# Optimization experiments

Hardware: AMD Instinct MI355X
Metric: run time of the kernel (lower is better)

Reference implementation:

```python
import jax, jax.numpy as jnp
import numpy as np

VOXEL_LENGTH = 1.2


def grid_sample_3d_border(vol, grid):
    """torch.nn.functional.grid_sample (5D, bilinear, align_corners=False,
    padding_mode='border') with grid flattened to (B, N, 3) in (x, y, z) order.
    vol: (B, C, D, H, W). Returns (B, C, N)."""

    def sample_one(v, g):
        C, D, H, W = v.shape
        x, y, z = g[:, 0], g[:, 1], g[:, 2]
        # align_corners=False unnormalization
        ix = ((x + 1.0) * W - 1.0) * 0.5
        iy = ((y + 1.0) * H - 1.0) * 0.5
        iz = ((z + 1.0) * D - 1.0) * 0.5
        ix0f, iy0f, iz0f = jnp.floor(ix), jnp.floor(iy), jnp.floor(iz)
        wx, wy, wz = ix - ix0f, iy - iy0f, iz - iz0f
        # border padding: clamp indices, keep unclamped weights
        x0 = jnp.clip(ix0f, 0, W - 1).astype(jnp.int32)
        x1 = jnp.clip(ix0f + 1, 0, W - 1).astype(jnp.int32)
        y0 = jnp.clip(iy0f, 0, H - 1).astype(jnp.int32)
        y1 = jnp.clip(iy0f + 1, 0, H - 1).astype(jnp.int32)
        z0 = jnp.clip(iz0f, 0, D - 1).astype(jnp.int32)
        z1 = jnp.clip(iz0f + 1, 0, D - 1).astype(jnp.int32)
        vflat = v.reshape(C, D * H * W)

        def gather(zi, yi, xi):  # -> (C, N)
            return vflat[:, (zi * H + yi) * W + xi]

        out = (
            gather(z0, y0, x0) * ((1 - wz) * (1 - wy) * (1 - wx))
            + gather(z0, y0, x1) * ((1 - wz) * (1 - wy) * wx)
            + gather(z0, y1, x0) * ((1 - wz) * wy * (1 - wx))
            + gather(z0, y1, x1) * ((1 - wz) * wy * wx)
            + gather(z1, y0, x0) * (wz * (1 - wy) * (1 - wx))
            + gather(z1, y0, x1) * (wz * (1 - wy) * wx)
            + gather(z1, y1, x0) * (wz * wy * (1 - wx))
            + gather(z1, y1, x1) * (wz * wy * wx)
        )
        return out

    return jax.vmap(sample_one)(vol, grid)


def setup_inputs() -> dict:
    key = jax.random.key(0)
    ks = jax.random.split(key, 16)
    B, IMG, STEPS = 2, 64, 24
    N = IMG * IMG * STEPS
    C_IN, HID, RES = 32, 256, 32
    # points in world space, inside the voxel cube [-0.6, 0.6]
    points = jax.random.uniform(ks[0], (B, N, 3), jnp.float32) * 1.2 - 0.6
    feature_volume = jax.random.normal(ks[1], (B, C_IN, RES, RES, RES), jnp.float32)

    def lin(k, fan_in, fan_out, scale):
        kw, kb = jax.random.split(k)
        W = jax.random.uniform(kw, (fan_out, fan_in), jnp.float32, -scale, scale)
        b = jax.random.uniform(kb, (fan_out,), jnp.float32, -scale, scale)
        return W, b

    freq = 12.0
    W0, b0 = lin(ks[2], C_IN, HID, 1.0 / C_IN)  # first_layer_film_sine_init
    W1, b1 = lin(ks[3], HID, HID, float(np.sqrt(6.0 / HID) / freq))
    W2, b2 = lin(ks[4], HID, HID, float(np.sqrt(6.0 / HID) / freq))
    W3, b3 = lin(ks[5], HID, HID, float(np.sqrt(6.0 / HID) / freq))
    Wf, bf = lin(ks[6], HID, 4, float(np.sqrt(6.0 / HID) / freq))
    return {
        "points": points, "feature_volume": feature_volume,
        "W0": W0, "b0": b0, "W1": W1, "b1": b1, "W2": W2, "b2": b2,
        "W3": W3, "b3": b3, "Wf": Wf, "bf": bf,
        "img_size": 64, "num_steps": 24,
    }


def reference(points, feature_volume, W0, b0, W1, b1, W2, b2, W3, b3, Wf, bf,
              img_size, num_steps):
    grid = points / (VOXEL_LENGTH / 2.0)  # (B, N, 3) in [-1, 1]
    feats = grid_sample_3d_border(feature_volume, grid)  # (B, C, N)
    x = feats.transpose(0, 2, 1)  # (B, N, C)
    for W, b in ((W0, b0), (W1, b1), (W2, b2), (W3, b3)):
        x = jnp.sin(jnp.einsum('bnc,hc->bnh', x, W) + b)
    rgb_sigma = jnp.einsum('bnh,oh->bno', x, Wf) + bf  # (B, N, 4)
    rgb = jax.nn.sigmoid(rgb_sigma[..., :3])
    sigma = rgb_sigma[..., 3:4]
    return jnp.concatenate([rgb, sigma], axis=-1)
```

## Files before the change

kernel.cpp:

```cpp
#include <hip/hip_runtime.h>
#include <math.h>

#define THREADS 256

typedef __attribute__((ext_vector_type(8))) short bf16x8;
typedef __attribute__((ext_vector_type(4))) float f32x4;

#define STREAM_BYTES  458752

__device__ __host__ __forceinline__ int sigma_k(int k) {
    return (k & 0xE1) | ((k & 0x04) << 2) | ((k & 0x18) >> 1) | (k & 0x02);
}

__device__ __forceinline__ ushort f2bf(float f) {
    union { float f; unsigned u; } v; v.f = f;
    unsigned r = v.u + 0x7FFFu + ((v.u >> 16) & 1u);
    return (ushort)(r >> 16);
}

__device__ __forceinline__ float fast_sigmoid(float x) {
    return 1.0f / (1.0f + __expf(-x));
}

__device__ __forceinline__ unsigned cvt_pk_bf16(float lo, float hi) {
    unsigned d;
    asm("v_cvt_pk_bf16_f32 %0, %1, %2" : "=v"(d) : "v"(lo), "v"(hi));
    return d;
}

__global__ void build_frags(const float* __restrict__ W0,
                            const float* __restrict__ W1,
                            const float* __restrict__ W2,
                            const float* __restrict__ W3,
                            const float* __restrict__ Wf,
                            ushort* __restrict__ stream) {
    const int gid = blockIdx.x * 256 + threadIdx.x;
    const int f = gid >> 6;
    const int lane = gid & 63;
    const int p16 = lane & 15, g = lane >> 4;
    ushort* dst = stream + (size_t)f * 512 + lane * 8;

    if (f < 16) {
        const float* row = W0 + (size_t)(f * 16 + p16) * 32;
#pragma unroll
        for (int i = 0; i < 8; ++i) dst[i] = f2bf(row[8 * g + i]);
    } else if (f < 32) {
#pragma unroll
        for (int i = 0; i < 8; ++i) dst[i] = 0;
    } else if (f < 416) {
        const int t = f - 32;
        const int h = t >> 7;
        const int q = (t >> 5) & 3;
        const int ksl = (t >> 3) & 3;
        const int ntl = t & 7;
        const int nt = (q & 1) * 8 + ntl;
        const int ks = (q >> 1) * 4 + ksl;
        const float* W = (h == 0) ? W1 : (h == 1) ? W2 : W3;
        const float* row = W + (size_t)(nt * 16 + p16) * 256;
#pragma unroll
        for (int i = 0; i < 8; ++i) dst[i] = f2bf(row[sigma_k(32 * ks + 8 * g + i)]);
    } else if (f < 424) {
        const int ks = f - 416;
        if (p16 < 4) {
            const float* row = Wf + (size_t)p16 * 256;
#pragma unroll
            for (int i = 0; i < 8; ++i) dst[i] = f2bf(row[sigma_k(32 * ks + 8 * g + i)]);
        } else {
#pragma unroll
            for (int i = 0; i < 8; ++i) dst[i] = 0;
        }
    } else {
#pragma unroll
        for (int i = 0; i < 8; ++i) dst[i] = 0;
    }
}

__global__ void vol_chlast(const float* __restrict__ vol, float* __restrict__ dst, int nvox) {
    int v = blockIdx.x * 256 + threadIdx.x;
    if (v >= nvox) return;
    const int b = v >> 15, idx = v & 32767;
    const float* s = vol + (size_t)b * 32 * 32768 + idx;
    float* d = dst + (size_t)v * 32;
#pragma unroll
    for (int c = 0; c < 32; ++c) d[c] = s[(size_t)c * 32768];
}

#define MF(a, b, c) __builtin_amdgcn_mfma_f32_16x16x32_bf16((a), (b), (c), 0, 0, 0)

__global__ __launch_bounds__(THREADS, 2)
void siren_pl(const float* __restrict__ points,
              const float* __restrict__ vol,
              const float* __restrict__ b0, const float* __restrict__ b1,
              const float* __restrict__ b2, const float* __restrict__ b3,
              const float* __restrict__ bfin,
              const ushort* __restrict__ Wstream,
              const float* __restrict__ volcl, int use_cl,
              float* __restrict__ out, long long total, int N) {
    __shared__ ushort ring[2][16384];

    const int tid = (int)threadIdx.x;
    const int w = tid >> 6;
    const int lane = tid & 63;
    const int p16 = lane & 15;
    const int g = lane >> 4;

    const long long base = (long long)blockIdx.x * 128;

    auto stage = [&](int c) {
        if (c >= 14) return;
        const ushort* src = Wstream + (size_t)c * 16384;
        ushort* dstbase = &ring[c & 1][0];
#pragma unroll
        for (int q = 0; q < 8; ++q) {
            const int off = (q * 4 + w) * 512;
            __builtin_amdgcn_global_load_lds(
                (const __attribute__((address_space(1))) unsigned int*)(src + off + lane * 8),
                (__attribute__((address_space(3))) unsigned int*)(dstbase + off),
                16, 0, 0);
        }
    };
    stage(0);
    stage(1);

    bf16x8 af0[2];
    {
#pragma unroll
        for (int ptt = 0; ptt < 2; ++ptt) {
            const long long gidx = base + w * 32 + ptt * 16 + p16;
            const long long gp = gidx < total ? gidx : total - 1;
            const int bi = (int)(gp / N);
            const float* pp = points + gp * 3;
            const float sc = 1.0f / 0.6f;
            const float ix = (pp[0] * sc + 1.0f) * 16.0f - 0.5f;
            const float iy = (pp[1] * sc + 1.0f) * 16.0f - 0.5f;
            const float iz = (pp[2] * sc + 1.0f) * 16.0f - 0.5f;
            const float fx = floorf(ix), fy = floorf(iy), fz = floorf(iz);
            const float wx = ix - fx, wy = iy - fy, wz = iz - fz;
            const int x0 = (int)fminf(fmaxf(fx, 0.0f), 31.0f);
            const int x1 = (int)fminf(fmaxf(fx + 1.0f, 0.0f), 31.0f);
            const int y0 = (int)fminf(fmaxf(fy, 0.0f), 31.0f);
            const int y1 = (int)fminf(fmaxf(fy + 1.0f, 0.0f), 31.0f);
            const int z0 = (int)fminf(fmaxf(fz, 0.0f), 31.0f);
            const int z1 = (int)fminf(fmaxf(fz + 1.0f, 0.0f), 31.0f);
            const int i000 = (z0 * 32 + y0) * 32 + x0, i001 = (z0 * 32 + y0) * 32 + x1;
            const int i010 = (z0 * 32 + y1) * 32 + x0, i011 = (z0 * 32 + y1) * 32 + x1;
            const int i100 = (z1 * 32 + y0) * 32 + x0, i101 = (z1 * 32 + y0) * 32 + x1;
            const int i110 = (z1 * 32 + y1) * 32 + x0, i111 = (z1 * 32 + y1) * 32 + x1;
            const float omx = 1.0f - wx, omy = 1.0f - wy, omz = 1.0f - wz;
            const float w000 = omz * omy * omx, w001 = omz * omy * wx;
            const float w010 = omz * wy * omx,  w011 = omz * wy * wx;
            const float w100 = wz * omy * omx,  w101 = wz * omy * wx;
            const float w110 = wz * wy * omx,   w111 = wz * wy * wx;

            f32x4 a[2];
            if (use_cl) {
                const float* vb = volcl + (size_t)bi * 32768 * 32 + g * 8;
#pragma unroll
                for (int h = 0; h < 2; ++h) {
                    const float* vh = vb + h * 4;
                    a[h]  = w000 * *(const f32x4*)(vh + (size_t)i000 * 32);
                    a[h] += w001 * *(const f32x4*)(vh + (size_t)i001 * 32);
                    a[h] += w010 * *(const f32x4*)(vh + (size_t)i010 * 32);
                    a[h] += w011 * *(const f32x4*)(vh + (size_t)i011 * 32);
                    a[h] += w100 * *(const f32x4*)(vh + (size_t)i100 * 32);
                    a[h] += w101 * *(const f32x4*)(vh + (size_t)i101 * 32);
                    a[h] += w110 * *(const f32x4*)(vh + (size_t)i110 * 32);
                    a[h] += w111 * *(const f32x4*)(vh + (size_t)i111 * 32);
                }
            } else {
                const float* vb = vol + ((size_t)bi * 32 + (size_t)g * 8) * 32768;
#pragma unroll
                for (int c = 0; c < 8; ++c) {
                    const float* vc = vb + (size_t)c * 32768;
                    a[c >> 2][c & 3] =
                        vc[i000] * w000 + vc[i001] * w001 + vc[i010] * w010 + vc[i011] * w011 +
                        vc[i100] * w100 + vc[i101] * w101 + vc[i110] * w110 + vc[i111] * w111;
                }
            }
            union { bf16x8 v; unsigned u[4]; } pk;
            pk.u[0] = cvt_pk_bf16(a[0][0], a[0][1]);
            pk.u[1] = cvt_pk_bf16(a[0][2], a[0][3]);
            pk.u[2] = cvt_pk_bf16(a[1][0], a[1][1]);
            pk.u[3] = cvt_pk_bf16(a[1][2], a[1][3]);
            af0[ptt] = pk.v;
        }
    }

    f32x4 accA[2][8];
    f32x4 accB[2][8];
    bf16x8 bfr[2][8];

    auto frag_at = [&](int slot, int idx) -> bf16x8 {
        return *(const bf16x8*)&ring[slot][idx * 512 + lane * 8];
    };
    auto init_half = [&](f32x4 (&A)[2][8], const float* __restrict__ b, int ntbase) {
#pragma unroll
        for (int m = 0; m < 8; ++m) {
            const f32x4 bv = *(const f32x4*)&b[(ntbase + m) * 16 + 4 * g];
            A[0][m] = bv; A[1][m] = bv;
        }
    };
    auto pack_half = [&](f32x4 (&A)[2][8], int ksbase) {
#pragma unroll
        for (int ptt = 0; ptt < 2; ++ptt)
#pragma unroll
            for (int ks2 = 0; ks2 < 4; ++ks2) {
                union { bf16x8 v; unsigned u[4]; } pk;
#pragma unroll
                for (int j = 0; j < 4; ++j) {
                    const int m = 2 * ks2 + (j >> 1);
                    const int r = 2 * (j & 1);
                    pk.u[j] = cvt_pk_bf16(__sinf(A[ptt][m][r]), __sinf(A[ptt][m][r + 1]));
                }
                bfr[ptt][ksbase + ks2] = pk.v;
            }
    };
    auto chunk_mfma = [&](int slot, int kh, f32x4 (&A)[2][8]) {
        __builtin_amdgcn_s_setprio(1);
#pragma unroll
        for (int ksl = 0; ksl < 4; ++ksl) {
            const bf16x8 bA = bfr[0][kh * 4 + ksl];
            const bf16x8 bB = bfr[1][kh * 4 + ksl];
#pragma unroll
            for (int ntl = 0; ntl < 8; ++ntl) {
                const bf16x8 wfr = frag_at(slot, ksl * 8 + ntl);
                A[0][ntl] = MF(wfr, bA, A[0][ntl]);
                A[1][ntl] = MF(wfr, bB, A[1][ntl]);
            }
        }
        __builtin_amdgcn_s_setprio(0);
    };

    init_half(accA, b0, 0);
    init_half(accB, b0, 8);
    __syncthreads();

    __builtin_amdgcn_s_setprio(1);
#pragma unroll
    for (int ntl = 0; ntl < 8; ++ntl) {
        const bf16x8 wl = frag_at(0, ntl);
        const bf16x8 wh = frag_at(0, 8 + ntl);
        accA[0][ntl] = MF(wl, af0[0], accA[0][ntl]);
        accA[1][ntl] = MF(wl, af0[1], accA[1][ntl]);
        accB[0][ntl] = MF(wh, af0[0], accB[0][ntl]);
        accB[1][ntl] = MF(wh, af0[1], accB[1][ntl]);
    }
    __builtin_amdgcn_s_setprio(0);
    __syncthreads(); stage(2);

    pack_half(accA, 0); init_half(accA, b1, 0);
    chunk_mfma(1, 0, accA);
    __syncthreads(); stage(3);
    pack_half(accB, 4); init_half(accB, b1, 8);
    chunk_mfma(0, 0, accB);
    __syncthreads(); stage(4);
    chunk_mfma(1, 1, accA);
    __syncthreads(); stage(5);
    pack_half(accA, 0); init_half(accA, b2, 0);
    chunk_mfma(0, 1, accB);
    __syncthreads(); stage(6);
    pack_half(accB, 4); init_half(accB, b2, 8);
    chunk_mfma(1, 0, accA);
    __syncthreads(); stage(7);
    chunk_mfma(0, 0, accB);
    __syncthreads(); stage(8);
    chunk_mfma(1, 1, accA);
    __syncthreads(); stage(9);
    pack_half(accA, 0); init_half(accA, b3, 0);
    chunk_mfma(0, 1, accB);
    __syncthreads(); stage(10);
    pack_half(accB, 4); init_half(accB, b3, 8);
    chunk_mfma(1, 0, accA);
    __syncthreads(); stage(11);
    chunk_mfma(0, 0, accB);
    __syncthreads(); stage(12);
    chunk_mfma(1, 1, accA);
    __syncthreads(); stage(13);
    pack_half(accA, 0);
    chunk_mfma(0, 1, accB);
    __syncthreads();
    pack_half(accB, 4);
    {
        f32x4 fo[2] = {{0, 0, 0, 0}, {0, 0, 0, 0}};
#pragma unroll
        for (int ks = 0; ks < 8; ++ks) {
            const bf16x8 wfr = frag_at(1, ks);
            fo[0] = MF(wfr, bfr[0][ks], fo[0]);
            fo[1] = MF(wfr, bfr[1][ks], fo[1]);
        }
        if (g == 0) {
#pragma unroll
            for (int ptt = 0; ptt < 2; ++ptt) {
                const long long oi = base + w * 32 + ptt * 16 + p16;
                if (oi < total) {
                    float4 o;
                    o.x = fast_sigmoid(fo[ptt][0] + bfin[0]);
                    o.y = fast_sigmoid(fo[ptt][1] + bfin[1]);
                    o.z = fast_sigmoid(fo[ptt][2] + bfin[2]);
                    o.w = fo[ptt][3] + bfin[3];
                    *(float4*)(out + oi * 4) = o;
                }
            }
        }
    }
}

extern "C" void kernel_launch(void* const* d_in, const int* in_sizes, int n_in,
                              void* d_out, int out_size, void* d_ws, size_t ws_size,
                              hipStream_t stream) {
    const float* points = (const float*)d_in[0];
    const float* vol    = (const float*)d_in[1];
    const float* W0 = (const float*)d_in[2];
    const float* b0 = (const float*)d_in[3];
    const float* W1 = (const float*)d_in[4];
    const float* b1 = (const float*)d_in[5];
    const float* W2 = (const float*)d_in[6];
    const float* b2 = (const float*)d_in[7];
    const float* W3 = (const float*)d_in[8];
    const float* b3 = (const float*)d_in[9];
    const float* Wf = (const float*)d_in[10];
    const float* bf = (const float*)d_in[11];

    const int B = in_sizes[1] / (32 * 32 * 32 * 32);
    const int N = in_sizes[0] / (3 * B);
    const long long total = (long long)B * N;
    const int tiles = (int)((total + 127) / 128);

    ushort* Wstream = (ushort*)d_ws;
    build_frags<<<112, 256, 0, stream>>>(W0, W1, W2, W3, Wf, Wstream);

    const int use_cl = (ws_size >= (size_t)STREAM_BYTES + (size_t)B * 32768 * 32 * 4) ? 1 : 0;
    float* volcl = (float*)((char*)d_ws + STREAM_BYTES);
    if (use_cl) {
        const int nvox = B * 32768;
        vol_chlast<<<(nvox + 255) / 256, 256, 0, stream>>>(vol, volcl, nvox);
    }

    siren_pl<<<tiles, THREADS, 0, stream>>>(
        points, vol, b0, b1, b2, b3, bf, Wstream, volcl, use_cl,
        (float*)d_out, total, N);
}
```

Baseline: 107.7 us.

## Double points per block to 256 and reuse each weight fragment across four tiles

```diff
diff --git a/kernel.cpp b/kernel.cpp
--- a/kernel.cpp
+++ b/kernel.cpp
@@ -87,7 +87,7 @@
 
 #define MF(a, b, c) __builtin_amdgcn_mfma_f32_16x16x32_bf16((a), (b), (c), 0, 0, 0)
 
-__global__ __launch_bounds__(THREADS, 2)
+__global__ __launch_bounds__(THREADS, 1)
 void siren_pl(const float* __restrict__ points,
               const float* __restrict__ vol,
               const float* __restrict__ b0, const float* __restrict__ b1,
@@ -104,7 +104,7 @@
     const int p16 = lane & 15;
     const int g = lane >> 4;
 
-    const long long base = (long long)blockIdx.x * 128;
+    const long long base = (long long)blockIdx.x * 256;
 
     auto stage = [&](int c) {
         if (c >= 14) return;
@@ -122,11 +122,11 @@
     stage(0);
     stage(1);
 
-    bf16x8 af0[2];
+    bf16x8 af0[4];
     {
 #pragma unroll
-        for (int ptt = 0; ptt < 2; ++ptt) {
-            const long long gidx = base + w * 32 + ptt * 16 + p16;
+        for (int ptt = 0; ptt < 4; ++ptt) {
+            const long long gidx = base + w * 64 + ptt * 16 + p16;
             const long long gp = gidx < total ? gidx : total - 1;
             const int bi = (int)(gp / N);
             const float* pp = points + gp * 3;
@@ -186,23 +186,24 @@
         }
     }
 
-    f32x4 accA[2][8];
-    f32x4 accB[2][8];
-    bf16x8 bfr[2][8];
+    f32x4 accA[4][8];
+    f32x4 accB[4][8];
+    bf16x8 bfr[4][8];
 
     auto frag_at = [&](int slot, int idx) -> bf16x8 {
         return *(const bf16x8*)&ring[slot][idx * 512 + lane * 8];
     };
-    auto init_half = [&](f32x4 (&A)[2][8], const float* __restrict__ b, int ntbase) {
+    auto init_half = [&](f32x4 (&A)[4][8], const float* __restrict__ b, int ntbase) {
 #pragma unroll
         for (int m = 0; m < 8; ++m) {
             const f32x4 bv = *(const f32x4*)&b[(ntbase + m) * 16 + 4 * g];
-            A[0][m] = bv; A[1][m] = bv;
-        }
-    };
-    auto pack_half = [&](f32x4 (&A)[2][8], int ksbase) {
-#pragma unroll
-        for (int ptt = 0; ptt < 2; ++ptt)
+#pragma unroll
+            for (int ptt = 0; ptt < 4; ++ptt) A[ptt][m] = bv;
+        }
+    };
+    auto pack_half = [&](f32x4 (&A)[4][8], int ksbase) {
+#pragma unroll
+        for (int ptt = 0; ptt < 4; ++ptt)
 #pragma unroll
             for (int ks2 = 0; ks2 < 4; ++ks2) {
                 union { bf16x8 v; unsigned u[4]; } pk;
@@ -215,37 +216,33 @@
                 bfr[ptt][ksbase + ks2] = pk.v;
             }
     };
-    auto chunk_mfma = [&](int slot, int kh, f32x4 (&A)[2][8]) {
-        __builtin_amdgcn_s_setprio(1);
+    auto chunk_mfma = [&](int slot, int kh, f32x4 (&A)[4][8]) {
 #pragma unroll
         for (int ksl = 0; ksl < 4; ++ksl) {
-            const bf16x8 bA = bfr[0][kh * 4 + ksl];
-            const bf16x8 bB = bfr[1][kh * 4 + ksl];
 #pragma unroll
             for (int ntl = 0; ntl < 8; ++ntl) {
                 const bf16x8 wfr = frag_at(slot, ksl * 8 + ntl);
-                A[0][ntl] = MF(wfr, bA, A[0][ntl]);
-                A[1][ntl] = MF(wfr, bB, A[1][ntl]);
+#pragma unroll
+                for (int ptt = 0; ptt < 4; ++ptt)
+                    A[ptt][ntl] = MF(wfr, bfr[ptt][kh * 4 + ksl], A[ptt][ntl]);
             }
         }
-        __builtin_amdgcn_s_setprio(0);
     };
 
     init_half(accA, b0, 0);
     init_half(accB, b0, 8);
     __syncthreads();
 
-    __builtin_amdgcn_s_setprio(1);
 #pragma unroll
     for (int ntl = 0; ntl < 8; ++ntl) {
         const bf16x8 wl = frag_at(0, ntl);
         const bf16x8 wh = frag_at(0, 8 + ntl);
-        accA[0][ntl] = MF(wl, af0[0], accA[0][ntl]);
-        accA[1][ntl] = MF(wl, af0[1], accA[1][ntl]);
-        accB[0][ntl] = MF(wh, af0[0], accB[0][ntl]);
-        accB[1][ntl] = MF(wh, af0[1], accB[1][ntl]);
-    }
-    __builtin_amdgcn_s_setprio(0);
+#pragma unroll
+        for (int ptt = 0; ptt < 4; ++ptt) {
+            accA[ptt][ntl] = MF(wl, af0[ptt], accA[ptt][ntl]);
+            accB[ptt][ntl] = MF(wh, af0[ptt], accB[ptt][ntl]);
+        }
+    }
     __syncthreads(); stage(2);
 
     pack_half(accA, 0); init_half(accA, b1, 0);
@@ -281,17 +278,18 @@
     __syncthreads();
     pack_half(accB, 4);
     {
-        f32x4 fo[2] = {{0, 0, 0, 0}, {0, 0, 0, 0}};
+        f32x4 fo[4] = {{0,0,0,0}, {0,0,0,0}, {0,0,0,0}, {0,0,0,0}};
 #pragma unroll
         for (int ks = 0; ks < 8; ++ks) {
             const bf16x8 wfr = frag_at(1, ks);
-            fo[0] = MF(wfr, bfr[0][ks], fo[0]);
-            fo[1] = MF(wfr, bfr[1][ks], fo[1]);
+#pragma unroll
+            for (int ptt = 0; ptt < 4; ++ptt)
+                fo[ptt] = MF(wfr, bfr[ptt][ks], fo[ptt]);
         }
         if (g == 0) {
 #pragma unroll
-            for (int ptt = 0; ptt < 2; ++ptt) {
-                const long long oi = base + w * 32 + ptt * 16 + p16;
+            for (int ptt = 0; ptt < 4; ++ptt) {
+                const long long oi = base + w * 64 + ptt * 16 + p16;
                 if (oi < total) {
                     float4 o;
                     o.x = fast_sigmoid(fo[ptt][0] + bfin[0]);
@@ -324,7 +322,7 @@
     const int B = in_sizes[1] / (32 * 32 * 32 * 32);
     const int N = in_sizes[0] / (3 * B);
     const long long total = (long long)B * N;
-    const int tiles = (int)((total + 127) / 128);
+    const int tiles = (int)((total + 255) / 256);
 
     ushort* Wstream = (ushort*)d_ws;
     build_frags<<<112, 256, 0, stream>>>(W0, W1, W2, W3, Wf, Wstream);
```

New measurement: 142.0 us. +31.9%, slower.

## Read MFMA weight fragments directly from global memory instead of LDS ring

Applied to the files above, without the earlier changes.

```diff
diff --git a/kernel.cpp b/kernel.cpp
--- a/kernel.cpp
+++ b/kernel.cpp
@@ -96,8 +96,6 @@
               const ushort* __restrict__ Wstream,
               const float* __restrict__ volcl, int use_cl,
               float* __restrict__ out, long long total, int N) {
-    __shared__ ushort ring[2][16384];
-
     const int tid = (int)threadIdx.x;
     const int w = tid >> 6;
     const int lane = tid & 63;
@@ -106,21 +104,7 @@
 
     const long long base = (long long)blockIdx.x * 128;
 
-    auto stage = [&](int c) {
-        if (c >= 14) return;
-        const ushort* src = Wstream + (size_t)c * 16384;
-        ushort* dstbase = &ring[c & 1][0];
-#pragma unroll
-        for (int q = 0; q < 8; ++q) {
-            const int off = (q * 4 + w) * 512;
-            __builtin_amdgcn_global_load_lds(
-                (const __attribute__((address_space(1))) unsigned int*)(src + off + lane * 8),
-                (__attribute__((address_space(3))) unsigned int*)(dstbase + off),
-                16, 0, 0);
-        }
-    };
-    stage(0);
-    stage(1);
+    const bf16x8* __restrict__ fragp = (const bf16x8*)Wstream + lane;
 
     bf16x8 af0[2];
     {
@@ -190,9 +174,6 @@
     f32x4 accB[2][8];
     bf16x8 bfr[2][8];
 
-    auto frag_at = [&](int slot, int idx) -> bf16x8 {
-        return *(const bf16x8*)&ring[slot][idx * 512 + lane * 8];
-    };
     auto init_half = [&](f32x4 (&A)[2][8], const float* __restrict__ b, int ntbase) {
 #pragma unroll
         for (int m = 0; m < 8; ++m) {
@@ -215,7 +196,7 @@
                 bfr[ptt][ksbase + ks2] = pk.v;
             }
     };
-    auto chunk_mfma = [&](int slot, int kh, f32x4 (&A)[2][8]) {
+    auto sub_mfma = [&](int fbase, int kh, f32x4 (&A)[2][8]) {
         __builtin_amdgcn_s_setprio(1);
 #pragma unroll
         for (int ksl = 0; ksl < 4; ++ksl) {
@@ -223,7 +204,7 @@
             const bf16x8 bB = bfr[1][kh * 4 + ksl];
 #pragma unroll
             for (int ntl = 0; ntl < 8; ++ntl) {
-                const bf16x8 wfr = frag_at(slot, ksl * 8 + ntl);
+                const bf16x8 wfr = fragp[(fbase + ksl * 8 + ntl) * 64];
                 A[0][ntl] = MF(wfr, bA, A[0][ntl]);
                 A[1][ntl] = MF(wfr, bB, A[1][ntl]);
             }
@@ -233,58 +214,40 @@
 
     init_half(accA, b0, 0);
     init_half(accB, b0, 8);
-    __syncthreads();
-
     __builtin_amdgcn_s_setprio(1);
 #pragma unroll
     for (int ntl = 0; ntl < 8; ++ntl) {
-        const bf16x8 wl = frag_at(0, ntl);
-        const bf16x8 wh = frag_at(0, 8 + ntl);
-        accA[0][ntl] = MF(wl, af0[0], accA[0][ntl]);
-        accA[1][ntl] = MF(wl, af0[1], accA[1][ntl]);
-        accB[0][ntl] = MF(wh, af0[0], accB[0][ntl]);
-        accB[1][ntl] = MF(wh, af0[1], accB[1][ntl]);
+        const bf16x8 wl = fragp[ntl * 64];
+        const bf16x8 wh = fragp[(8 + ntl) * 64];
+#pragma unroll
+        for (int ptt = 0; ptt < 2; ++ptt) {
+            accA[ptt][ntl] = MF(wl, af0[ptt], accA[ptt][ntl]);
+            accB[ptt][ntl] = MF(wh, af0[ptt], accB[ptt][ntl]);
+        }
     }
     __builtin_amdgcn_s_setprio(0);
-    __syncthreads(); stage(2);
-
-    pack_half(accA, 0); init_half(accA, b1, 0);
-    chunk_mfma(1, 0, accA);
-    __syncthreads(); stage(3);
-    pack_half(accB, 4); init_half(accB, b1, 8);
-    chunk_mfma(0, 0, accB);
-    __syncthreads(); stage(4);
-    chunk_mfma(1, 1, accA);
-    __syncthreads(); stage(5);
-    pack_half(accA, 0); init_half(accA, b2, 0);
-    chunk_mfma(0, 1, accB);
-    __syncthreads(); stage(6);
-    pack_half(accB, 4); init_half(accB, b2, 8);
-    chunk_mfma(1, 0, accA);
-    __syncthreads(); stage(7);
-    chunk_mfma(0, 0, accB);
-    __syncthreads(); stage(8);
-    chunk_mfma(1, 1, accA);
-    __syncthreads(); stage(9);
-    pack_half(accA, 0); init_half(accA, b3, 0);
-    chunk_mfma(0, 1, accB);
-    __syncthreads(); stage(10);
-    pack_half(accB, 4); init_half(accB, b3, 8);
-    chunk_mfma(1, 0, accA);
-    __syncthreads(); stage(11);
-    chunk_mfma(0, 0, accB);
-    __syncthreads(); stage(12);
-    chunk_mfma(1, 1, accA);
-    __syncthreads(); stage(13);
+
+#define LAYER(F, BNEXT)                                                \
+    do {                                                               \
+        pack_half(accA, 0); init_half(accA, BNEXT, 0);                 \
+        sub_mfma((F), 0, accA);                                        \
+        pack_half(accB, 4); init_half(accB, BNEXT, 8);                 \
+        sub_mfma((F) + 32, 0, accB);                                   \
+        sub_mfma((F) + 64, 1, accA);                                   \
+        sub_mfma((F) + 96, 1, accB);                                   \
+    } while (0)
+
+    LAYER(32, b1);
+    LAYER(160, b2);
+    LAYER(288, b3);
+
     pack_half(accA, 0);
-    chunk_mfma(0, 1, accB);
-    __syncthreads();
     pack_half(accB, 4);
     {
         f32x4 fo[2] = {{0, 0, 0, 0}, {0, 0, 0, 0}};
 #pragma unroll
         for (int ks = 0; ks < 8; ++ks) {
-            const bf16x8 wfr = frag_at(1, ks);
+            const bf16x8 wfr = fragp[(416 + ks) * 64];
             fo[0] = MF(wfr, bfr[0][ks], fo[0]);
             fo[1] = MF(wfr, bfr[1][ks], fo[1]);
         }
```

Result: slower. 199.0 us (+84.8%).
